# Optimization experiments

Measured on AMD Instinct MI355X. Metric: run time of the kernel, lower is better.

## Reference

```python
import jax, jax.numpy as jnp
import numpy as np

N_HEADS = 16

def setup_inputs() -> dict:
    key = jax.random.key(0)
    ks = jax.random.split(key, 5)
    B, T, C = 4, 2048, 1024
    s = 0.02
    return {
        "x": jax.random.normal(ks[0], (B, T, C), jnp.float32),
        "W_attn": jax.random.normal(ks[1], (C, 3 * C), jnp.float32) * s,
        "b_attn": jax.random.normal(ks[2], (3 * C,), jnp.float32) * s,
        "W_proj": jax.random.normal(ks[3], (C, C), jnp.float32) * s,
        "b_proj": jax.random.normal(ks[4], (C,), jnp.float32) * s,
    }

def reference(x, W_attn, b_attn, W_proj, b_proj):
    B, T, C = x.shape
    H = N_HEADS
    D = C // H  # head dim
    qkv = x @ W_attn + b_attn                      # [B,T,3C]
    q, k, v = jnp.split(qkv, 3, axis=2)
    # [B,T,C] -> [B,H,T,D]
    q = q.reshape(B, T, H, D).transpose(0, 2, 1, 3)
    k = k.reshape(B, T, H, D).transpose(0, 2, 1, 3)
    v = v.reshape(B, T, H, D).transpose(0, 2, 1, 3)
    scale = 1.0 / jnp.sqrt(jnp.asarray(D, q.dtype))
    attn = jnp.einsum("bhqd,bhkd->bhqk", q, k) * scale  # [B,H,T,T]
    causal = jnp.tril(jnp.ones((T, T), bool))
    attn = jnp.where(causal[None, None], attn, -jnp.inf)
    attn = jax.nn.softmax(attn, axis=-1)
    y = jnp.einsum("bhqk,bhkd->bhqd", attn, v)          # [B,H,T,D]
    y = y.transpose(0, 2, 1, 3).reshape(B, T, C)
    return y @ W_proj + b_proj
```

## Files before the change

kernel.cpp:

```cpp
#include <hip/hip_runtime.h>

typedef __bf16 bf16x8 __attribute__((ext_vector_type(8)));
typedef float f32x4 __attribute__((ext_vector_type(4)));
typedef float f32x16 __attribute__((ext_vector_type(16)));
typedef unsigned short ushort8 __attribute__((ext_vector_type(8)));
typedef unsigned int uint4v __attribute__((ext_vector_type(4)));

__device__ __forceinline__ unsigned short f2bf(float f) {
  __bf16 b = (__bf16)f;
  return __builtin_bit_cast(unsigned short, b);
}
__device__ __forceinline__ float bf2f(unsigned short u) {
  unsigned int x = ((unsigned int)u) << 16;
  return __builtin_bit_cast(float, x);
}

#define GLOAD_LDS16(g, l)                                              \
  __builtin_amdgcn_global_load_lds(                                    \
      (const __attribute__((address_space(1))) void*)(g),              \
      (__attribute__((address_space(3))) void*)(l), 16, 0, 0)

__global__ __launch_bounds__(256) void f32_to_bf16_kernel(const float* __restrict__ in,
                                                          __bf16* __restrict__ out) {
  int i = blockIdx.x * 256 + threadIdx.x;
  const float4* p = (const float4*)(in + (size_t)i * 8);
  float4 f0 = p[0], f1 = p[1];
  ushort8 u = {f2bf(f0.x), f2bf(f0.y), f2bf(f0.z), f2bf(f0.w),
               f2bf(f1.x), f2bf(f1.y), f2bf(f1.z), f2bf(f1.w)};
  *(ushort8*)((unsigned short*)out + (size_t)i * 8) = u;
}

__global__ __launch_bounds__(256) void wtrans_kernel(const float* __restrict__ W,
                                                     __bf16* __restrict__ Wt,
                                                     int K, int N) {
  __shared__ float tile[32][33];
  int tx = threadIdx.x, ty = threadIdx.y;
  int n0 = blockIdx.x * 32, k0 = blockIdx.y * 32;
#pragma unroll
  for (int i = 0; i < 32; i += 8)
    tile[ty + i][tx] = W[(size_t)(k0 + ty + i) * N + n0 + tx];
  __syncthreads();
#pragma unroll
  for (int i = 0; i < 32; i += 8)
    Wt[(size_t)(n0 + ty + i) * K + k0 + tx] = (__bf16)tile[tx][ty + i];
}

template <int OUT_F32, int KSPLIT>
__global__ __launch_bounds__(512, 2) void gemm256_kernel(const __bf16* __restrict__ Ab,
                                                         const __bf16* __restrict__ Bt,
                                                         const float* __restrict__ bias,
                                                         void* __restrict__ Cp,
                                                         __bf16* __restrict__ Kbp,
                                                         int M, int N, int K) {
  __shared__ __align__(16) unsigned short As[2][256 * 64];
  __shared__ __align__(16) unsigned short Bs[2][128 * 64];
  const int tid = threadIdx.x;
  const int lane = tid & 63;
  const int wid = tid >> 6;
  const int lr = lane & 15, lg = lane >> 4;
  const int wr = wid >> 1, wc = wid & 1;
  const int gx = gridDim.x;
  int nwg = gx * gridDim.y;
  int bid = blockIdx.y * gx + blockIdx.x;
  if ((nwg & 7) == 0) {
    int cpx = nwg >> 3;
    bid = (bid & 7) * cpx + (bid >> 3);
  }
  const int m0 = (bid / gx) * 256, n0 = (bid % gx) * 128;
  const int srow = tid >> 3;
  const int scol = ((tid & 7) ^ (srow & 7)) * 8;
  const unsigned short* Ag = (const unsigned short*)Ab + (size_t)(m0 + srow) * K + scol;
  const unsigned short* Bg = (const unsigned short*)Bt + (size_t)(n0 + srow) * K + scol;

#define STAGE256(t, bi)                                                      \
  {                                                                          \
    const int _k0 = (t) * 64;                                                \
    GLOAD_LDS16(Ag + _k0, &As[bi][tid * 8]);                                 \
    GLOAD_LDS16(Ag + (size_t)64 * K + _k0, &As[bi][4096 + tid * 8]);         \
    GLOAD_LDS16(Ag + (size_t)128 * K + _k0, &As[bi][8192 + tid * 8]);        \
    GLOAD_LDS16(Ag + (size_t)192 * K + _k0, &As[bi][12288 + tid * 8]);       \
    GLOAD_LDS16(Bg + _k0, &Bs[bi][tid * 8]);                                 \
    GLOAD_LDS16(Bg + (size_t)64 * K + _k0, &Bs[bi][4096 + tid * 8]);         \
  }

  f32x4 acc[4][4] = {};
  const int nst = K >> 6;
  STAGE256(0, 0);
  STAGE256(1, 1);
  int aoff[4][2], boff[4][2];
#pragma unroll
  for (int t = 0; t < 4; ++t)
#pragma unroll
    for (int ks = 0; ks < 2; ++ks) {
      int slot = ((ks * 4 + lg) ^ (lr & 7));
      aoff[t][ks] = (wr * 64 + t * 16 + lr) * 64 + slot * 8;
      boff[t][ks] = (wc * 64 + t * 16 + lr) * 64 + slot * 8;
    }

  for (int i = 0; i < nst; ++i) {
    const int cur = i & 1;
    if (i + 1 < nst)
      asm volatile("s_waitcnt vmcnt(6)" ::: "memory");
    else
      asm volatile("s_waitcnt vmcnt(0)" ::: "memory");
    asm volatile("s_barrier" ::: "memory");
    bf16x8 af[4][2], bq[4][2];
#pragma unroll
    for (int t = 0; t < 4; ++t)
#pragma unroll
      for (int ks = 0; ks < 2; ++ks) {
        af[t][ks] = *(const bf16x8*)&As[cur][aoff[t][ks]];
        bq[t][ks] = *(const bf16x8*)&Bs[cur][boff[t][ks]];
      }
    asm volatile("s_waitcnt lgkmcnt(0)" ::: "memory");
    asm volatile("s_barrier" ::: "memory");
    if (i + 2 < nst) STAGE256(i + 2, cur);
    __builtin_amdgcn_s_setprio(1);
#pragma unroll
    for (int mt = 0; mt < 4; ++mt)
#pragma unroll
      for (int nt = 0; nt < 4; ++nt)
#pragma unroll
        for (int ks = 0; ks < 2; ++ks)
          acc[mt][nt] =
              __builtin_amdgcn_mfma_f32_16x16x32_bf16(af[mt][ks], bq[nt][ks], acc[mt][nt], 0, 0, 0);
    __builtin_amdgcn_s_setprio(0);
  }
#undef STAGE256

  const bool isK = KSPLIT && (n0 >= 1024) && (n0 < 2048);
#pragma unroll
  for (int mt = 0; mt < 4; ++mt)
#pragma unroll
    for (int nt = 0; nt < 4; ++nt)
#pragma unroll
      for (int jj = 0; jj < 4; ++jj) {
        int row = m0 + wr * 64 + mt * 16 + lg * 4 + jj;
        int col = n0 + wc * 64 + nt * 16 + lr;
        float v = acc[mt][nt][jj] + bias[col];
        if (OUT_F32) {
          ((float*)Cp)[(size_t)row * N + col] = v;
        } else if (isK) {
          int h = (col - 1024) >> 6, d = col & 63;
          int bq2 = row >> 11, t = row & 2047;
          ((unsigned short*)Kbp)[(size_t)((bq2 * 16 + h) * 2048 + t) * 64 + d] = f2bf(v);
        } else {
          ((unsigned short*)Cp)[(size_t)row * N + col] = f2bf(v);
        }
      }
}

__global__ __launch_bounds__(256) void vtrans_kernel(const __bf16* __restrict__ qkv,
                                                     __bf16* __restrict__ Vt) {
  __shared__ __align__(16) unsigned short tile[64][72];
  int bh = blockIdx.y, b = bh >> 4, h = bh & 15;
  int t0 = blockIdx.x * 64;
  int tid = threadIdx.x;
#pragma unroll
  for (int p = 0; p < 2; ++p) {
    int idx = p * 256 + tid;
    int r = idx >> 3, c8 = (idx & 7) * 8;
    *(ushort8*)&tile[r][c8] = *(const ushort8*)((const unsigned short*)qkv +
                                                (size_t)(b * 2048 + t0 + r) * 3072 + 2048 +
                                                h * 64 + c8);
  }
  __syncthreads();
#pragma unroll
  for (int p = 0; p < 2; ++p) {
    int idx = p * 256 + tid;
    int d = idx >> 3, c8 = (idx & 7) * 8;
    ushort8 u;
#pragma unroll
    for (int i = 0; i < 8; ++i) u[i] = tile[c8 + i][d];
    *(ushort8*)((unsigned short*)Vt + (size_t)(bh * 64 + d) * 2048 + t0 + c8) = u;
  }
}

__global__ __launch_bounds__(512) void attn_kernel(const __bf16* __restrict__ qkvp,
                                                   const __bf16* __restrict__ Kg,
                                                   const __bf16* __restrict__ Vt,
                                                   __bf16* __restrict__ yb) {
  __shared__ __align__(16) unsigned short Ks[2][64][72];
  __shared__ __align__(16) unsigned short Vs[2][64][72];
  const int bx = blockIdx.x;
  const int qb = 7 - (bx >> 6);
  const int bh = bx & 63;
  const int b = bh >> 4, h = bh & 15;
  const int tid = threadIdx.x, wid = tid >> 6, lane = tid & 63;
  const int lq = lane & 31, hi = lane >> 5;
  const unsigned short* qkv = (const unsigned short*)qkvp;
  const unsigned short* Kh = (const unsigned short*)Kg + (size_t)bh * 2048 * 64;
  const unsigned short* Vh = (const unsigned short*)Vt + (size_t)bh * 64 * 2048;
  const int q0w = qb * 256 + wid * 32;
  const int jmax_w = 4 * qb + (wid >> 1);
  const int qrel = (wid & 1) * 32 + lq;
  const int J = 4 * qb + 4;
  const int r = tid >> 3, c8s = (tid & 7) * 8;

  const float qs = 0.125f * 1.44269504f;
  bf16x8 qf[4];
  {
    const unsigned short* Qg = qkv + (size_t)(b * 2048 + q0w + lq) * 3072 + h * 64;
#pragma unroll
    for (int dc = 0; dc < 4; ++dc) {
      ushort8 uq = *(const ushort8*)(Qg + dc * 16 + hi * 8);
      uint4v w;
#pragma unroll
      for (int i = 0; i < 4; ++i) {
        float lo = bf2f(uq[2 * i]) * qs;
        float hh = bf2f(uq[2 * i + 1]) * qs;
        unsigned int up;
        asm("v_cvt_pk_bf16_f32 %0, %1, %2" : "=v"(up) : "v"(lo), "v"(hh));
        w[i] = up;
      }
      qf[dc] = __builtin_bit_cast(bf16x8, w);
    }
  }

  f32x16 yacc[2] = {};
  float m_r = -1e30f, l_r = 0.f;

  *(ushort8*)&Ks[0][r][c8s] = *(const ushort8*)(Kh + (size_t)r * 64 + c8s);
  *(ushort8*)&Vs[0][r][c8s] = *(const ushort8*)(Vh + (size_t)r * 2048 + c8s);

  for (int j = 0; j < J; ++j) {
    __syncthreads();
    if (j + 1 < J) {
      int bi = (j + 1) & 1;
      *(ushort8*)&Ks[bi][r][c8s] =
          *(const ushort8*)(Kh + (size_t)((j + 1) * 64 + r) * 64 + c8s);
      *(ushort8*)&Vs[bi][r][c8s] =
          *(const ushort8*)(Vh + (size_t)r * 2048 + (j + 1) * 64 + c8s);
    }
    if (j <= jmax_w) {
      const int cb = j & 1;
      f32x16 sa[2];
#pragma unroll
      for (int kt32 = 0; kt32 < 2; ++kt32) {
        f32x16 s = {};
#pragma unroll
        for (int dc = 0; dc < 4; ++dc) {
          bf16x8 kf = *(const bf16x8*)&Ks[cb][kt32 * 32 + lq][dc * 16 + hi * 8];
          s = __builtin_amdgcn_mfma_f32_32x32x16_bf16(kf, qf[dc], s, 0, 0, 0);
        }
        sa[kt32] = s;
      }
      if (j == jmax_w) {
#pragma unroll
        for (int kt32 = 0; kt32 < 2; ++kt32)
#pragma unroll
          for (int reg = 0; reg < 16; ++reg) {
            int kl = kt32 * 32 + (reg & 3) + 8 * (reg >> 2) + 4 * hi;
            if (kl > qrel) sa[kt32][reg] = -1e30f;
          }
      }
      float pmax = -1e30f;
#pragma unroll
      for (int kt32 = 0; kt32 < 2; ++kt32)
#pragma unroll
        for (int reg = 0; reg < 16; reg += 4)
          pmax = fmaxf(pmax, fmaxf(fmaxf(sa[kt32][reg], sa[kt32][reg + 1]),
                                   fmaxf(sa[kt32][reg + 2], sa[kt32][reg + 3])));
      pmax = fmaxf(pmax, __shfl_xor(pmax, 32));
      const bool need = __any(pmax > m_r + 8.f) != 0;
      const float mnew = need ? fmaxf(m_r, pmax) : m_r;
      const float alpha = exp2f(m_r - mnew);
      unsigned int u[2][8];
      float rs = 0.f;
#pragma unroll
      for (int kt32 = 0; kt32 < 2; ++kt32)
#pragma unroll
        for (int rr = 0; rr < 8; ++rr) {
          float p0 = exp2f(sa[kt32][2 * rr] - mnew);
          float p1 = exp2f(sa[kt32][2 * rr + 1] - mnew);
          rs += p0 + p1;
          unsigned int up;
          asm("v_cvt_pk_bf16_f32 %0, %1, %2" : "=v"(up) : "v"(p0), "v"(p1));
          u[kt32][rr] = up;
        }
      rs += __shfl_xor(rs, 32);
      l_r = l_r * alpha + rs;
      m_r = mnew;
      if (need) {
#pragma unroll
        for (int reg = 0; reg < 16; ++reg) {
          int row = (reg & 3) + 8 * (reg >> 2) + 4 * hi;
          float ac = __shfl(alpha, row);
          yacc[0][reg] *= ac;
          yacc[1][reg] *= ac;
        }
      }
#pragma unroll
      for (int kt = 0; kt < 4; ++kt) {
        const int kt32 = kt >> 1, off = 4 * (kt & 1);
        unsigned int a0 = u[kt32][off + 0], a2 = u[kt32][off + 2];
        unsigned int a1 = u[kt32][off + 1], a3 = u[kt32][off + 3];
        asm("v_permlane32_swap_b32 %0, %1" : "+v"(a0), "+v"(a2));
        asm("v_permlane32_swap_b32 %0, %1" : "+v"(a1), "+v"(a3));
        uint4v pav = {a0, a1, a2, a3};
        bf16x8 paf = __builtin_bit_cast(bf16x8, pav);
#pragma unroll
        for (int dt = 0; dt < 2; ++dt) {
          bf16x8 vf = *(const bf16x8*)&Vs[cb][dt * 32 + lq][kt * 16 + hi * 8];
          yacc[dt] = __builtin_amdgcn_mfma_f32_32x32x16_bf16(paf, vf, yacc[dt], 0, 0, 0);
        }
      }
    }
  }
#pragma unroll
  for (int reg = 0; reg < 16; ++reg) {
    int row = (reg & 3) + 8 * (reg >> 2) + 4 * hi;
    float linv = 1.f / __shfl(l_r, row);
    int qg = q0w + row;
#pragma unroll
    for (int dt = 0; dt < 2; ++dt) {
      float v = yacc[dt][reg] * linv;
      ((unsigned short*)yb)[(size_t)(b * 2048 + qg) * 1024 + h * 64 + dt * 32 + lq] = f2bf(v);
    }
  }
}

extern "C" void kernel_launch(void* const* d_in, const int* in_sizes, int n_in,
                              void* d_out, int out_size, void* d_ws, size_t ws_size,
                              hipStream_t stream) {
  const float* x = (const float*)d_in[0];
  const float* W_attn = (const float*)d_in[1];
  const float* b_attn = (const float*)d_in[2];
  const float* W_proj = (const float*)d_in[3];
  const float* b_proj = (const float*)d_in[4];
  float* out = (float*)d_out;
  char* ws = (char*)d_ws;

  size_t off = 0;
  __bf16* WtA = (__bf16*)(ws + off); off += (size_t)3072 * 1024 * 2;
  __bf16* WtP = (__bf16*)(ws + off); off += (size_t)1024 * 1024 * 2;
  __bf16* qkv = (__bf16*)(ws + off); off += (size_t)8192 * 3072 * 2;
  __bf16* Kb  = (__bf16*)(ws + off); off += (size_t)64 * 2048 * 64 * 2;
  __bf16* Vtb = (__bf16*)(ws + off); off += (size_t)64 * 2048 * 64 * 2;
  __bf16* xyb = (__bf16*)(ws + off); off += (size_t)8192 * 1024 * 2;
  __bf16* xb = xyb;
  __bf16* yb = xyb;
  (void)ws_size; (void)in_sizes; (void)n_in; (void)out_size;

  f32_to_bf16_kernel<<<4096, 256, 0, stream>>>(x, xb);
  wtrans_kernel<<<dim3(3072 / 32, 1024 / 32), dim3(32, 8), 0, stream>>>(W_attn, WtA, 1024, 3072);
  wtrans_kernel<<<dim3(1024 / 32, 1024 / 32), dim3(32, 8), 0, stream>>>(W_proj, WtP, 1024, 1024);
  gemm256_kernel<0, 1><<<dim3(24, 32), 512, 0, stream>>>(xb, WtA, b_attn, qkv, Kb, 8192, 3072, 1024);
  vtrans_kernel<<<dim3(32, 64), 256, 0, stream>>>(qkv, Vtb);
  attn_kernel<<<dim3(512), 512, 0, stream>>>(qkv, Kb, Vtb, yb);
  gemm256_kernel<1, 0><<<dim3(8, 32), 512, 0, stream>>>(yb, WtP, b_proj, out, nullptr, 8192, 1024, 1024);
}
```

Measured before the change: 192.2 us.

## Add 256x256-tile ping-pong GEMM with staged half-tile loads for QKV projection

Adds a new GEMM kernel for the QKV projection. It uses 256x256 output tiles across 8 waves, with each wave owning a 128x64 sub-block. Each K-step is split into four MFMA phases, and the next half-tile A/B global-to-LDS loads are interleaved between them, separated by barriers. The larger tile is meant to raise arithmetic intensity and to overlap loads with compute better. In exchange it uses more LDS and registers and adds more barriers per K-step, and the grid shrinks to 384 workgroups. The existing GEMM also gets a minor change to hoist its LDS base pointers.

Result: slower. 199.6 us (+3.8%).

```diff
diff --git a/kernel.cpp b/kernel.cpp
--- a/kernel.cpp
+++ b/kernel.cpp
@@ -43,6 +43,171 @@
 #pragma unroll
   for (int i = 0; i < 32; i += 8)
     Wt[(size_t)(n0 + ty + i) * K + k0 + tx] = (__bf16)tile[tx][ty + i];
+}
+
+template <int KSPLIT>
+__global__ __launch_bounds__(512, 2) void gemm8p_kernel(const __bf16* __restrict__ Ab,
+                                                        const __bf16* __restrict__ Bt,
+                                                        const float* __restrict__ bias,
+                                                        void* __restrict__ Cp,
+                                                        __bf16* __restrict__ Kbp,
+                                                        int M, int N, int K) {
+  __shared__ __align__(16) unsigned short As[2][2][128 * 64];
+  __shared__ __align__(16) unsigned short Bs[2][2][128 * 64];
+  const int tid = threadIdx.x;
+  const int lane = tid & 63, wid = tid >> 6;
+  const int lr = lane & 15, lg = lane >> 4;
+  const int wr = wid >> 2, wc = wid & 3;
+  const int gx = gridDim.x;
+  int nwg = gx * gridDim.y;
+  int bid = blockIdx.y * gx + blockIdx.x;
+  if ((nwg & 7) == 0) {
+    int cpx = nwg >> 3;
+    bid = (bid & 7) * cpx + (bid >> 3);
+  }
+  const int m0 = (bid / gx) * 256, n0 = (bid % gx) * 256;
+  const int nst = K >> 6;
+  const int srow = tid >> 3;
+  const int scol = ((tid & 7) ^ (srow & 7)) * 8;
+  const unsigned short* Ag = (const unsigned short*)Ab + (size_t)(m0 + srow) * K + scol;
+  const unsigned short* Bg = (const unsigned short*)Bt + (size_t)(n0 + srow) * K + scol;
+
+#define STA(t, h)                                                               \
+  {                                                                             \
+    int _tc = ((t) < nst) ? (t) : (nst - 1);                                    \
+    const unsigned short* _g = Ag + (size_t)(h) * 128 * K + _tc * 64;           \
+    unsigned short* _l = &As[(t) & 1][h][0];                                    \
+    GLOAD_LDS16(_g, _l + tid * 8);                                              \
+    GLOAD_LDS16(_g + (size_t)64 * K, _l + 4096 + tid * 8);                      \
+  }
+#define STB(t, h)                                                               \
+  {                                                                             \
+    int _tc = ((t) < nst) ? (t) : (nst - 1);                                    \
+    const unsigned short* _g = Bg + (size_t)(h) * 128 * K + _tc * 64;           \
+    unsigned short* _l = &Bs[(t) & 1][h][0];                                    \
+    GLOAD_LDS16(_g, _l + tid * 8);                                              \
+    GLOAD_LDS16(_g + (size_t)64 * K, _l + 4096 + tid * 8);                      \
+  }
+
+  f32x4 acc[8][4] = {};
+  const int xsw = lr & 7;
+
+  STA(0, 0); STA(0, 1); STB(0, 0); STB(0, 1); STB(1, 0); STB(1, 1);
+  asm volatile("s_waitcnt vmcnt(4)" ::: "memory");
+  asm volatile("s_barrier" ::: "memory");
+
+  for (int t = 0; t < nst; ++t) {
+    const int cur = t & 1;
+    bf16x8 a0[4][2], a1[4][2], b0[2][2], b1[2][2];
+#pragma unroll
+    for (int f = 0; f < 4; ++f)
+#pragma unroll
+      for (int ks = 0; ks < 2; ++ks)
+        a0[f][ks] = *(const bf16x8*)&As[cur][wr][(f * 16 + lr) * 64 +
+                                                 (((ks * 4 + lg) ^ xsw) * 8)];
+#pragma unroll
+    for (int g = 0; g < 2; ++g)
+#pragma unroll
+      for (int ks = 0; ks < 2; ++ks)
+        b0[g][ks] = *(const bf16x8*)&Bs[cur][wc >> 1][((wc & 1) * 64 + g * 16 + lr) * 64 +
+                                                      (((ks * 4 + lg) ^ xsw) * 8)];
+    STA(t + 1, 0);
+    asm volatile("s_waitcnt lgkmcnt(8)" ::: "memory");
+    asm volatile("s_barrier" ::: "memory");
+    asm volatile("s_waitcnt lgkmcnt(0)" ::: "memory");
+    __builtin_amdgcn_sched_barrier(0);
+    __builtin_amdgcn_s_setprio(1);
+#pragma unroll
+    for (int f = 0; f < 4; ++f)
+#pragma unroll
+      for (int g = 0; g < 2; ++g)
+#pragma unroll
+        for (int ks = 0; ks < 2; ++ks)
+          acc[f][g] = __builtin_amdgcn_mfma_f32_16x16x32_bf16(a0[f][ks], b0[g][ks], acc[f][g], 0, 0, 0);
+    __builtin_amdgcn_s_setprio(0);
+    asm volatile("s_barrier" ::: "memory");
+#pragma unroll
+    for (int g = 0; g < 2; ++g)
+#pragma unroll
+      for (int ks = 0; ks < 2; ++ks)
+        b1[g][ks] = *(const bf16x8*)&Bs[cur][wc >> 1][((wc & 1) * 64 + 32 + g * 16 + lr) * 64 +
+                                                      (((ks * 4 + lg) ^ xsw) * 8)];
+    STA(t + 1, 1);
+    asm volatile("s_barrier" ::: "memory");
+    asm volatile("s_waitcnt lgkmcnt(0)" ::: "memory");
+    __builtin_amdgcn_sched_barrier(0);
+    __builtin_amdgcn_s_setprio(1);
+#pragma unroll
+    for (int f = 0; f < 4; ++f)
+#pragma unroll
+      for (int g = 0; g < 2; ++g)
+#pragma unroll
+        for (int ks = 0; ks < 2; ++ks)
+          acc[f][2 + g] = __builtin_amdgcn_mfma_f32_16x16x32_bf16(a0[f][ks], b1[g][ks], acc[f][2 + g], 0, 0, 0);
+    __builtin_amdgcn_s_setprio(0);
+    asm volatile("s_barrier" ::: "memory");
+#pragma unroll
+    for (int f = 0; f < 4; ++f)
+#pragma unroll
+      for (int ks = 0; ks < 2; ++ks)
+        a1[f][ks] = *(const bf16x8*)&As[cur][wr][(64 + f * 16 + lr) * 64 +
+                                                 (((ks * 4 + lg) ^ xsw) * 8)];
+    STB(t + 2, 0);
+    asm volatile("s_barrier" ::: "memory");
+    asm volatile("s_waitcnt lgkmcnt(0)" ::: "memory");
+    __builtin_amdgcn_sched_barrier(0);
+    __builtin_amdgcn_s_setprio(1);
+#pragma unroll
+    for (int f = 0; f < 4; ++f)
+#pragma unroll
+      for (int g = 0; g < 2; ++g)
+#pragma unroll
+        for (int ks = 0; ks < 2; ++ks)
+          acc[4 + f][2 + g] = __builtin_amdgcn_mfma_f32_16x16x32_bf16(a1[f][ks], b1[g][ks], acc[4 + f][2 + g], 0, 0, 0);
+    __builtin_amdgcn_s_setprio(0);
+    asm volatile("s_barrier" ::: "memory");
+    STB(t + 2, 1);
+    asm volatile("s_barrier" ::: "memory");
+    __builtin_amdgcn_s_setprio(1);
+#pragma unroll
+    for (int f = 0; f < 4; ++f)
+#pragma unroll
+      for (int g = 0; g < 2; ++g)
+#pragma unroll
+        for (int ks = 0; ks < 2; ++ks)
+          acc[4 + f][g] = __builtin_amdgcn_mfma_f32_16x16x32_bf16(a1[f][ks], b0[g][ks], acc[4 + f][g], 0, 0, 0);
+    __builtin_amdgcn_s_setprio(0);
+    if (t >= nst - 2)
+      asm volatile("s_waitcnt vmcnt(0)" ::: "memory");
+    else
+      asm volatile("s_waitcnt vmcnt(4)" ::: "memory");
+    asm volatile("s_barrier" ::: "memory");
+  }
+#undef STA
+#undef STB
+
+  const bool isK = KSPLIT && (n0 >= 1024) && (n0 < 2048);
+#pragma unroll
+  for (int mh = 0; mh < 2; ++mh)
+#pragma unroll
+    for (int f = 0; f < 4; ++f)
+#pragma unroll
+      for (int nh = 0; nh < 2; ++nh)
+#pragma unroll
+        for (int g = 0; g < 2; ++g)
+#pragma unroll
+          for (int jj = 0; jj < 4; ++jj) {
+            int row = m0 + wr * 128 + mh * 64 + f * 16 + lg * 4 + jj;
+            int col = n0 + wc * 64 + nh * 32 + g * 16 + lr;
+            float v = acc[mh * 4 + f][nh * 2 + g][jj] + bias[col];
+            if (isK) {
+              int h = (col - 1024) >> 6, d = col & 63;
+              int bq2 = row >> 11, tt = row & 2047;
+              ((unsigned short*)Kbp)[(size_t)((bq2 * 16 + h) * 2048 + tt) * 64 + d] = f2bf(v);
+            } else {
+              ((unsigned short*)Cp)[(size_t)row * N + col] = f2bf(v);
+            }
+          }
 }
 
 template <int OUT_F32, int KSPLIT>
@@ -104,13 +269,15 @@
     else
       asm volatile("s_waitcnt vmcnt(0)" ::: "memory");
     asm volatile("s_barrier" ::: "memory");
+    const unsigned short* Ac = &As[cur][0];
+    const unsigned short* Bc = &Bs[cur][0];
     bf16x8 af[4][2], bq[4][2];
 #pragma unroll
     for (int t = 0; t < 4; ++t)
 #pragma unroll
       for (int ks = 0; ks < 2; ++ks) {
-        af[t][ks] = *(const bf16x8*)&As[cur][aoff[t][ks]];
-        bq[t][ks] = *(const bf16x8*)&Bs[cur][boff[t][ks]];
+        af[t][ks] = *(const bf16x8*)&Ac[aoff[t][ks]];
+        bq[t][ks] = *(const bf16x8*)&Bc[boff[t][ks]];
       }
     asm volatile("s_waitcnt lgkmcnt(0)" ::: "memory");
     asm volatile("s_barrier" ::: "memory");
@@ -345,7 +512,7 @@
   f32_to_bf16_kernel<<<4096, 256, 0, stream>>>(x, xb);
   wtrans_kernel<<<dim3(3072 / 32, 1024 / 32), dim3(32, 8), 0, stream>>>(W_attn, WtA, 1024, 3072);
   wtrans_kernel<<<dim3(1024 / 32, 1024 / 32), dim3(32, 8), 0, stream>>>(W_proj, WtP, 1024, 1024);
-  gemm256_kernel<0, 1><<<dim3(24, 32), 512, 0, stream>>>(xb, WtA, b_attn, qkv, Kb, 8192, 3072, 1024);
+  gemm8p_kernel<1><<<dim3(12, 32), 512, 0, stream>>>(xb, WtA, b_attn, qkv, Kb, 8192, 3072, 1024);
   vtrans_kernel<<<dim3(32, 64), 256, 0, stream>>>(qkv, Vtb);
   attn_kernel<<<dim3(512), 512, 0, stream>>>(qkv, Kb, Vtb, yb);
   gemm256_kernel<1, 0><<<dim3(8, 32), 512, 0, stream>>>(yb, WtP, b_proj, out, nullptr, 8192, 1024, 1024);
```

## Pair causal attention query blocks per workgroup to balance work

Applied to the files above, without the earlier changes.

Each attention workgroup now uses 256 threads and handles two 128-row query blocks, one near the start and its mirror near the end (p and 15-p). The pairing gives every workgroup the same amount of causal work and reuses each staged K/V tile for both blocks, so long-running tail blocks no longer dominate. The cost is twice the per-wave register state (two accumulators and two Q fragments) and each thread now loads two K/V chunks per tile. A small GEMM change hoists the LDS buffer base pointers out of the fragment loads.

Result: slower. 203.2 us (+5.7%).

```diff
diff --git a/kernel.cpp b/kernel.cpp
--- a/kernel.cpp
+++ b/kernel.cpp
@@ -104,13 +104,15 @@
     else
       asm volatile("s_waitcnt vmcnt(0)" ::: "memory");
     asm volatile("s_barrier" ::: "memory");
+    const unsigned short* Ac = &As[cur][0];
+    const unsigned short* Bc = &Bs[cur][0];
     bf16x8 af[4][2], bq[4][2];
 #pragma unroll
     for (int t = 0; t < 4; ++t)
 #pragma unroll
       for (int ks = 0; ks < 2; ++ks) {
-        af[t][ks] = *(const bf16x8*)&As[cur][aoff[t][ks]];
-        bq[t][ks] = *(const bf16x8*)&Bs[cur][boff[t][ks]];
+        af[t][ks] = *(const bf16x8*)&Ac[aoff[t][ks]];
+        bq[t][ks] = *(const bf16x8*)&Bc[boff[t][ks]];
       }
     asm volatile("s_waitcnt lgkmcnt(0)" ::: "memory");
     asm volatile("s_barrier" ::: "memory");
@@ -176,31 +178,31 @@
   }
 }
 
-__global__ __launch_bounds__(512) void attn_kernel(const __bf16* __restrict__ qkvp,
+__global__ __launch_bounds__(256) void attn_kernel(const __bf16* __restrict__ qkvp,
                                                    const __bf16* __restrict__ Kg,
                                                    const __bf16* __restrict__ Vt,
                                                    __bf16* __restrict__ yb) {
   __shared__ __align__(16) unsigned short Ks[2][64][72];
   __shared__ __align__(16) unsigned short Vs[2][64][72];
   const int bx = blockIdx.x;
-  const int qb = 7 - (bx >> 6);
+  const int p = bx >> 6;
   const int bh = bx & 63;
+  const int qbA = p, qbB = 15 - p;
   const int b = bh >> 4, h = bh & 15;
   const int tid = threadIdx.x, wid = tid >> 6, lane = tid & 63;
   const int lq = lane & 31, hi = lane >> 5;
   const unsigned short* qkv = (const unsigned short*)qkvp;
   const unsigned short* Kh = (const unsigned short*)Kg + (size_t)bh * 2048 * 64;
   const unsigned short* Vh = (const unsigned short*)Vt + (size_t)bh * 64 * 2048;
-  const int q0w = qb * 256 + wid * 32;
-  const int jmax_w = 4 * qb + (wid >> 1);
+  const int q0A = qbA * 128 + wid * 32, q0B = qbB * 128 + wid * 32;
+  const int jmaxA = 2 * qbA + (wid >> 1), jmaxB = 2 * qbB + (wid >> 1);
   const int qrel = (wid & 1) * 32 + lq;
-  const int J = 4 * qb + 4;
-  const int r = tid >> 3, c8s = (tid & 7) * 8;
+  const int J = 2 * qbB + 2;
 
   const float qs = 0.125f * 1.44269504f;
-  bf16x8 qf[4];
-  {
-    const unsigned short* Qg = qkv + (size_t)(b * 2048 + q0w + lq) * 3072 + h * 64;
+  bf16x8 qfA[4], qfB[4];
+  auto loadq = [&](int q0, bf16x8* qf) {
+    const unsigned short* Qg = qkv + (size_t)(b * 2048 + q0 + lq) * 3072 + h * 64;
 #pragma unroll
     for (int dc = 0; dc < 4; ++dc) {
       ushort8 uq = *(const ushort8*)(Qg + dc * 16 + hi * 8);
@@ -215,107 +217,127 @@
       }
       qf[dc] = __builtin_bit_cast(bf16x8, w);
     }
-  }
-
-  f32x16 yacc[2] = {};
-  float m_r = -1e30f, l_r = 0.f;
-
-  *(ushort8*)&Ks[0][r][c8s] = *(const ushort8*)(Kh + (size_t)r * 64 + c8s);
-  *(ushort8*)&Vs[0][r][c8s] = *(const ushort8*)(Vh + (size_t)r * 2048 + c8s);
+  };
+  loadq(q0A, qfA);
+  loadq(q0B, qfB);
+
+  f32x16 yaccA[2] = {}, yaccB[2] = {};
+  float mA = -1e30f, lA = 0.f, mB = -1e30f, lB = 0.f;
+
+  auto compute = [&](int j, int cb, int jmax, const bf16x8* qf, f32x16* yacc, float& m_r,
+                     float& l_r) {
+    f32x16 sa[2];
+#pragma unroll
+    for (int kt32 = 0; kt32 < 2; ++kt32) {
+      f32x16 s = {};
+#pragma unroll
+      for (int dc = 0; dc < 4; ++dc) {
+        bf16x8 kf = *(const bf16x8*)&Ks[cb][kt32 * 32 + lq][dc * 16 + hi * 8];
+        s = __builtin_amdgcn_mfma_f32_32x32x16_bf16(kf, qf[dc], s, 0, 0, 0);
+      }
+      sa[kt32] = s;
+    }
+    if (j == jmax) {
+#pragma unroll
+      for (int kt32 = 0; kt32 < 2; ++kt32)
+#pragma unroll
+        for (int reg = 0; reg < 16; ++reg) {
+          int kl = kt32 * 32 + (reg & 3) + 8 * (reg >> 2) + 4 * hi;
+          if (kl > qrel) sa[kt32][reg] = -1e30f;
+        }
+    }
+    float pmax = -1e30f;
+#pragma unroll
+    for (int kt32 = 0; kt32 < 2; ++kt32)
+#pragma unroll
+      for (int reg = 0; reg < 16; reg += 4)
+        pmax = fmaxf(pmax, fmaxf(fmaxf(sa[kt32][reg], sa[kt32][reg + 1]),
+                                 fmaxf(sa[kt32][reg + 2], sa[kt32][reg + 3])));
+    pmax = fmaxf(pmax, __shfl_xor(pmax, 32));
+    const bool need = __any(pmax > m_r + 8.f) != 0;
+    const float mnew = need ? fmaxf(m_r, pmax) : m_r;
+    const float alpha = exp2f(m_r - mnew);
+    unsigned int u[2][8];
+    float rs = 0.f;
+#pragma unroll
+    for (int kt32 = 0; kt32 < 2; ++kt32)
+#pragma unroll
+      for (int rr = 0; rr < 8; ++rr) {
+        float p0 = exp2f(sa[kt32][2 * rr] - mnew);
+        float p1 = exp2f(sa[kt32][2 * rr + 1] - mnew);
+        rs += p0 + p1;
+        unsigned int up;
+        asm("v_cvt_pk_bf16_f32 %0, %1, %2" : "=v"(up) : "v"(p0), "v"(p1));
+        u[kt32][rr] = up;
+      }
+    rs += __shfl_xor(rs, 32);
+    l_r = l_r * alpha + rs;
+    m_r = mnew;
+    if (need) {
+#pragma unroll
+      for (int reg = 0; reg < 16; ++reg) {
+        int row = (reg & 3) + 8 * (reg >> 2) + 4 * hi;
+        float ac = __shfl(alpha, row);
+        yacc[0][reg] *= ac;
+        yacc[1][reg] *= ac;
+      }
+    }
+#pragma unroll
+    for (int kt = 0; kt < 4; ++kt) {
+      const int kt32 = kt >> 1, off = 4 * (kt & 1);
+      unsigned int a0 = u[kt32][off + 0], a2 = u[kt32][off + 2];
+      unsigned int a1 = u[kt32][off + 1], a3 = u[kt32][off + 3];
+      asm("v_permlane32_swap_b32 %0, %1" : "+v"(a0), "+v"(a2));
+      asm("v_permlane32_swap_b32 %0, %1" : "+v"(a1), "+v"(a3));
+      uint4v pav = {a0, a1, a2, a3};
+      bf16x8 paf = __builtin_bit_cast(bf16x8, pav);
+#pragma unroll
+      for (int dt = 0; dt < 2; ++dt) {
+        bf16x8 vf = *(const bf16x8*)&Vs[cb][dt * 32 + lq][kt * 16 + hi * 8];
+        yacc[dt] = __builtin_amdgcn_mfma_f32_32x32x16_bf16(paf, vf, yacc[dt], 0, 0, 0);
+      }
+    }
+  };
+
+#pragma unroll
+  for (int pp = 0; pp < 2; ++pp) {
+    int idx = pp * 256 + tid;
+    int r = idx >> 3, c8 = (idx & 7) * 8;
+    *(ushort8*)&Ks[0][r][c8] = *(const ushort8*)(Kh + (size_t)r * 64 + c8);
+    *(ushort8*)&Vs[0][r][c8] = *(const ushort8*)(Vh + (size_t)r * 2048 + c8);
+  }
 
   for (int j = 0; j < J; ++j) {
     __syncthreads();
     if (j + 1 < J) {
       int bi = (j + 1) & 1;
-      *(ushort8*)&Ks[bi][r][c8s] =
-          *(const ushort8*)(Kh + (size_t)((j + 1) * 64 + r) * 64 + c8s);
-      *(ushort8*)&Vs[bi][r][c8s] =
-          *(const ushort8*)(Vh + (size_t)r * 2048 + (j + 1) * 64 + c8s);
-    }
-    if (j <= jmax_w) {
-      const int cb = j & 1;
-      f32x16 sa[2];
-#pragma unroll
-      for (int kt32 = 0; kt32 < 2; ++kt32) {
-        f32x16 s = {};
-#pragma unroll
-        for (int dc = 0; dc < 4; ++dc) {
-          bf16x8 kf = *(const bf16x8*)&Ks[cb][kt32 * 32 + lq][dc * 16 + hi * 8];
-          s = __builtin_amdgcn_mfma_f32_32x32x16_bf16(kf, qf[dc], s, 0, 0, 0);
-        }
-        sa[kt32] = s;
-      }
-      if (j == jmax_w) {
-#pragma unroll
-        for (int kt32 = 0; kt32 < 2; ++kt32)
-#pragma unroll
-          for (int reg = 0; reg < 16; ++reg) {
-            int kl = kt32 * 32 + (reg & 3) + 8 * (reg >> 2) + 4 * hi;
-            if (kl > qrel) sa[kt32][reg] = -1e30f;
-          }
-      }
-      float pmax = -1e30f;
-#pragma unroll
-      for (int kt32 = 0; kt32 < 2; ++kt32)
-#pragma unroll
-        for (int reg = 0; reg < 16; reg += 4)
-          pmax = fmaxf(pmax, fmaxf(fmaxf(sa[kt32][reg], sa[kt32][reg + 1]),
-                                   fmaxf(sa[kt32][reg + 2], sa[kt32][reg + 3])));
-      pmax = fmaxf(pmax, __shfl_xor(pmax, 32));
-      const bool need = __any(pmax > m_r + 8.f) != 0;
-      const float mnew = need ? fmaxf(m_r, pmax) : m_r;
-      const float alpha = exp2f(m_r - mnew);
-      unsigned int u[2][8];
-      float rs = 0.f;
-#pragma unroll
-      for (int kt32 = 0; kt32 < 2; ++kt32)
-#pragma unroll
-        for (int rr = 0; rr < 8; ++rr) {
-          float p0 = exp2f(sa[kt32][2 * rr] - mnew);
-          float p1 = exp2f(sa[kt32][2 * rr + 1] - mnew);
-          rs += p0 + p1;
-          unsigned int up;
-          asm("v_cvt_pk_bf16_f32 %0, %1, %2" : "=v"(up) : "v"(p0), "v"(p1));
-          u[kt32][rr] = up;
-        }
-      rs += __shfl_xor(rs, 32);
-      l_r = l_r * alpha + rs;
-      m_r = mnew;
-      if (need) {
-#pragma unroll
-        for (int reg = 0; reg < 16; ++reg) {
-          int row = (reg & 3) + 8 * (reg >> 2) + 4 * hi;
-          float ac = __shfl(alpha, row);
-          yacc[0][reg] *= ac;
-          yacc[1][reg] *= ac;
-        }
-      }
-#pragma unroll
-      for (int kt = 0; kt < 4; ++kt) {
-        const int kt32 = kt >> 1, off = 4 * (kt & 1);
-        unsigned int a0 = u[kt32][off + 0], a2 = u[kt32][off + 2];
-        unsigned int a1 = u[kt32][off + 1], a3 = u[kt32][off + 3];
-        asm("v_permlane32_swap_b32 %0, %1" : "+v"(a0), "+v"(a2));
-        asm("v_permlane32_swap_b32 %0, %1" : "+v"(a1), "+v"(a3));
-        uint4v pav = {a0, a1, a2, a3};
-        bf16x8 paf = __builtin_bit_cast(bf16x8, pav);
-#pragma unroll
-        for (int dt = 0; dt < 2; ++dt) {
-          bf16x8 vf = *(const bf16x8*)&Vs[cb][dt * 32 + lq][kt * 16 + hi * 8];
-          yacc[dt] = __builtin_amdgcn_mfma_f32_32x32x16_bf16(paf, vf, yacc[dt], 0, 0, 0);
-        }
-      }
-    }
-  }
+#pragma unroll
+      for (int pp = 0; pp < 2; ++pp) {
+        int idx = pp * 256 + tid;
+        int r = idx >> 3, c8 = (idx & 7) * 8;
+        *(ushort8*)&Ks[bi][r][c8] =
+            *(const ushort8*)(Kh + (size_t)((j + 1) * 64 + r) * 64 + c8);
+        *(ushort8*)&Vs[bi][r][c8] =
+            *(const ushort8*)(Vh + (size_t)r * 2048 + (j + 1) * 64 + c8);
+      }
+    }
+    const int cb = j & 1;
+    if (j <= jmaxA) compute(j, cb, jmaxA, qfA, yaccA, mA, lA);
+    if (j <= jmaxB) compute(j, cb, jmaxB, qfB, yaccB, mB, lB);
+  }
+
 #pragma unroll
   for (int reg = 0; reg < 16; ++reg) {
     int row = (reg & 3) + 8 * (reg >> 2) + 4 * hi;
-    float linv = 1.f / __shfl(l_r, row);
-    int qg = q0w + row;
+    float linvA = 1.f / __shfl(lA, row);
+    float linvB = 1.f / __shfl(lB, row);
+    int qgA = q0A + row, qgB = q0B + row;
 #pragma unroll
     for (int dt = 0; dt < 2; ++dt) {
-      float v = yacc[dt][reg] * linv;
-      ((unsigned short*)yb)[(size_t)(b * 2048 + qg) * 1024 + h * 64 + dt * 32 + lq] = f2bf(v);
+      float vA = yaccA[dt][reg] * linvA;
+      float vB = yaccB[dt][reg] * linvB;
+      ((unsigned short*)yb)[(size_t)(b * 2048 + qgA) * 1024 + h * 64 + dt * 32 + lq] = f2bf(vA);
+      ((unsigned short*)yb)[(size_t)(b * 2048 + qgB) * 1024 + h * 64 + dt * 32 + lq] = f2bf(vB);
     }
   }
 }
@@ -347,6 +369,6 @@
   wtrans_kernel<<<dim3(1024 / 32, 1024 / 32), dim3(32, 8), 0, stream>>>(W_proj, WtP, 1024, 1024);
   gemm256_kernel<0, 1><<<dim3(24, 32), 512, 0, stream>>>(xb, WtA, b_attn, qkv, Kb, 8192, 3072, 1024);
   vtrans_kernel<<<dim3(32, 64), 256, 0, stream>>>(qkv, Vtb);
-  attn_kernel<<<dim3(512), 512, 0, stream>>>(qkv, Kb, Vtb, yb);
+  attn_kernel<<<dim3(512), 256, 0, stream>>>(qkv, Kb, Vtb, yb);
   gemm256_kernel<1, 0><<<dim3(8, 32), 512, 0, stream>>>(yb, WtP, b_proj, out, nullptr, 8192, 1024, 1024);
 }
```
